# Performance work log

Measured on AMD Instinct MI355X. Metric: run time of the kernel, lower is better.

Reference implementation:

```python
import jax, jax.numpy as jnp
import numpy as np

B, S, D, H = 2, 2048, 1024, 16
HD = D // H  # 64

def setup_inputs() -> dict:
    key = jax.random.key(0)
    k1, k2, k3 = jax.random.split(key, 3)
    hidden_states = jax.random.normal(k1, (B, S, D), dtype=jnp.float32)
    w_attn = jax.random.normal(k2, (D, 3 * D), dtype=jnp.float32) * 0.02
    w_proj = jax.random.normal(k3, (D, D), dtype=jnp.float32) * 0.02
    return {"hidden_states": hidden_states, "w_attn": w_attn, "w_proj": w_proj}

def reference(hidden_states, w_attn, w_proj):
    b, s, d = hidden_states.shape
    # c_attn: Conv1D (bias is a scalar zero in the source)
    qkv = jnp.einsum('bsd,de->bse', hidden_states, w_attn)  # [B,S,3D]
    q, k, v = jnp.split(qkv, 3, axis=-1)
    def split_heads(t):
        return t.reshape(b, s, H, HD).transpose(0, 2, 1, 3)  # [B,H,S,HD]
    q, k, v = split_heads(q), split_heads(k), split_heads(v)
    # eager attention; scale_attn_weights=True -> divide by sqrt(head_dim)
    scores = jnp.einsum('bhqd,bhkd->bhqk', q, k) / jnp.sqrt(jnp.float32(HD))
    # NOTE: source registers bias buffer as all-ones (True), so the causal
    # torch.where is a no-op -- faithfully no masking is applied.
    probs = jax.nn.softmax(scores, axis=-1)
    attn = jnp.einsum('bhqk,bhkd->bhqd', probs, v)  # [B,H,S,HD]
    attn = attn.transpose(0, 2, 1, 3).reshape(b, s, d)  # merge heads
    out = jnp.einsum('bsd,de->bse', attn, w_proj)  # c_proj (zero bias)
    return out
```

## Files before the change

### kernel.cpp

```cpp
#include <hip/hip_runtime.h>
#include <hip/hip_bf16.h>

typedef __attribute__((ext_vector_type(8))) short bf16x8;
typedef __attribute__((ext_vector_type(4))) short short4v;
typedef __attribute__((ext_vector_type(4))) float f32x4;
typedef __attribute__((ext_vector_type(16))) float f32x16;
typedef __attribute__((ext_vector_type(4))) float float4v;

__device__ __forceinline__ short f2bf(float f) {
    union { float f; unsigned u; } v; v.f = f;
    unsigned r = v.u + 0x7fffu + ((v.u >> 16) & 1u);
    return (short)(r >> 16);
}
__device__ __forceinline__ float bf2f(short s) {
    union { unsigned u; float f; } v;
    v.u = ((unsigned)(unsigned short)s) << 16;
    return v.f;
}

__device__ __forceinline__ void gload16(const short* g, short* lds) {
    __builtin_amdgcn_global_load_lds(
        (const __attribute__((address_space(1))) unsigned*)g,
        (__attribute__((address_space(3))) unsigned*)lds, 16, 0, 0);
}

__device__ __forceinline__ void tconv_tile(const float* __restrict__ in,
                                           short* __restrict__ out,
                                           int Kdim, int Ndim, int n0, int k0) {
    __shared__ int Ls[64][65];
    const int t = threadIdx.x;
    const int kl = t >> 4, n4 = (t & 15) * 4;
#pragma unroll
    for (int it = 0; it < 4; ++it) {
        int k = kl + it * 16;
        float4v v = *reinterpret_cast<const float4v*>(&in[(size_t)(k0 + k) * Ndim + n0 + n4]);
#pragma unroll
        for (int c = 0; c < 4; ++c) Ls[k][n4 + c] = (int)(unsigned short)f2bf(v[c]);
    }
    __syncthreads();
    const int nl0 = t >> 4, kq = (t & 15) * 4;
#pragma unroll
    for (int it = 0; it < 4; ++it) {
        int nl = nl0 + it * 16;
        short4v s;
#pragma unroll
        for (int j = 0; j < 4; ++j) s[j] = (short)Ls[kq + j][nl];
        *reinterpret_cast<short4v*>(&out[(size_t)(n0 + nl) * Kdim + k0 + kq]) = s;
    }
}

__global__ __launch_bounds__(256) void prep1(const float* __restrict__ hidden,
                                             short* __restrict__ Ah,
                                             const float* __restrict__ w_attn,
                                             short* __restrict__ Wta) {
    const int bx = blockIdx.x;
    if (bx < 2048) {
        int i = (bx * 256 + threadIdx.x) * 8;
        float4v a0 = *reinterpret_cast<const float4v*>(&hidden[i]);
        float4v a1 = *reinterpret_cast<const float4v*>(&hidden[i + 4]);
        bf16x8 s;
        s[0] = f2bf(a0[0]); s[1] = f2bf(a0[1]); s[2] = f2bf(a0[2]); s[3] = f2bf(a0[3]);
        s[4] = f2bf(a1[0]); s[5] = f2bf(a1[1]); s[6] = f2bf(a1[2]); s[7] = f2bf(a1[3]);
        *reinterpret_cast<bf16x8*>(&Ah[i]) = s;
    } else {
        int idx = bx - 2048;
        int n0 = (idx % 48) * 64, k0 = (idx / 48) * 64;
        tconv_tile(w_attn, Wta, 1024, 3072, n0, k0);
    }
}

__global__ __launch_bounds__(256) void qkv_gemm(const short* __restrict__ Ah,
                                                const short* __restrict__ Wt,
                                                short* __restrict__ Qw,
                                                short* __restrict__ Kw,
                                                short* __restrict__ Vt) {
    __shared__ short As[128 * 64];
    __shared__ short Bs[128 * 64];
    const int tid = threadIdx.x;
    const int l = tid & 63, w = tid >> 6;
    const int g = l >> 4, lr = l & 15;
    const int r8 = l >> 3, sl = l & 7;
    const int xs = (sl ^ r8) * 8;
    const int wm = (w >> 1) * 64, wn = (w & 1) * 64;
    const int bid = blockIdx.x;
    const int xcd = bid & 7, idx = bid >> 3;
    const int nt = (xcd & 1) * 12 + idx % 12;
    const int mt = (xcd >> 1) * 8 + idx / 12;
    const int m0 = mt * 128;
    const int n0 = nt * 128;
    const bool isV = (n0 >= 2048);
    f32x4 acc[4][4] = {};
    for (int k0 = 0; k0 < 1024; k0 += 64) {
        const short* Ag = Ah + m0 * 1024 + k0;
        const short* Bg = Wt + n0 * 1024 + k0;
#pragma unroll
        for (int i = 0; i < 4; ++i) {
            int seg = w * 4 + i;
            gload16(Ag + (seg * 8 + r8) * 1024 + xs, &As[seg * 512]);
            gload16(Bg + (seg * 8 + r8) * 1024 + xs, &Bs[seg * 512]);
        }
        __syncthreads();
#pragma unroll
        for (int kk = 0; kk < 2; ++kk) {
            bf16x8 af[4], bfr[4];
#pragma unroll
            for (int mi = 0; mi < 4; ++mi) {
                int row = wm + mi * 16 + lr;
                af[mi] = *reinterpret_cast<const bf16x8*>(&As[row * 64 + (((4 * kk + g) ^ (lr & 7)) * 8)]);
            }
#pragma unroll
            for (int ni = 0; ni < 4; ++ni) {
                int col = wn + ni * 16 + lr;
                bfr[ni] = *reinterpret_cast<const bf16x8*>(&Bs[col * 64 + (((4 * kk + g) ^ (lr & 7)) * 8)]);
            }
            if (isV) {
#pragma unroll
                for (int mi = 0; mi < 4; ++mi)
#pragma unroll
                    for (int ni = 0; ni < 4; ++ni)
                        acc[mi][ni] = __builtin_amdgcn_mfma_f32_16x16x32_bf16(af[mi], bfr[ni], acc[mi][ni], 0, 0, 0);
            } else {
#pragma unroll
                for (int mi = 0; mi < 4; ++mi)
#pragma unroll
                    for (int ni = 0; ni < 4; ++ni)
                        acc[mi][ni] = __builtin_amdgcn_mfma_f32_16x16x32_bf16(bfr[ni], af[mi], acc[mi][ni], 0, 0, 0);
            }
        }
        __syncthreads();
    }
    if (isV) {
#pragma unroll
        for (int mi = 0; mi < 4; ++mi) {
            int m = m0 + wm + mi * 16 + g * 4;
            int bb = m >> 11, s0 = m & 2047;
#pragma unroll
            for (int ni = 0; ni < 4; ++ni) {
                int n = n0 + wn + ni * 16 + lr;
                int hh = (n >> 6) & 15, d = n & 63;
                short4v pv;
#pragma unroll
                for (int r = 0; r < 4; ++r) pv[r] = f2bf(acc[mi][ni][r]);
                *reinterpret_cast<short4v*>(&Vt[(((bb * 16 + hh) * 64) + d) * 2048 + s0]) = pv;
            }
        }
    } else {
        const bool isQ = (n0 < 1024);
        const float sc = isQ ? 0.18033688011112042f : 1.0f;
        short* dst = isQ ? Qw : Kw;
#pragma unroll
        for (int mi = 0; mi < 4; ++mi) {
            int m = m0 + wm + mi * 16 + lr;
            int bb = m >> 11, s0 = m & 2047;
#pragma unroll
            for (int ni = 0; ni < 4; ++ni) {
                int n = n0 + wn + ni * 16 + g * 4;
                int hh = (n >> 6) & 15, d = n & 63;
                float a0 = acc[mi][ni][0] * sc, a1 = acc[mi][ni][1] * sc;
                float a2 = acc[mi][ni][2] * sc, a3 = acc[mi][ni][3] * sc;
                int w0, w1;
                asm("v_cvt_pk_bf16_f32 %0, %1, %2" : "=v"(w0) : "v"(a0), "v"(a1));
                asm("v_cvt_pk_bf16_f32 %0, %1, %2" : "=v"(w1) : "v"(a2), "v"(a3));
                union { int wd[2]; short4v s; } u;
                u.wd[0] = w0; u.wd[1] = w1;
                *reinterpret_cast<short4v*>(&dst[((bb * 16 + hh) * 2048 + s0) * 64 + d]) = u.s;
            }
        }
    }
}

__global__ __launch_bounds__(256, 4) void attn9(const short* __restrict__ Qw,
                                                const short* __restrict__ Kw,
                                                const short* __restrict__ Vt,
                                                short* __restrict__ N0,
                                                short* __restrict__ N1,
                                                float* __restrict__ Tot) {
    __shared__ short Ks[2][64 * 64];
    __shared__ short Vs[2][64 * 64];
    const int tid = threadIdx.x;
    const int w = tid >> 6, l = tid & 63;
    const int q = l & 31, hi = l >> 5;
    const int r8 = l >> 3, sl = l & 7;
    const int xs = (sl ^ r8) * 8;
    const int bid = blockIdx.x;
    const int work = (bid & 7) * 128 + (bid >> 3);
    const int head = work >> 5;
    const int qblk = (work & 31) >> 1;
    const int ks = work & 1;
    const int b = head >> 4, h = head & 15;
    const int q0 = qblk * 128 + w * 32;
    const short* Qb = Qw + ((b * 16 + h) * 2048 + q0) * 64;
    const short* Kb = Kw + ((b * 16 + h) * 2048 + ks * 1024) * 64;
    const short* Vb = Vt + ((b * 16 + h) * 64) * 2048 + ks * 1024;

    bf16x8 qb[4];
#pragma unroll
    for (int c = 0; c < 4; ++c)
        qb[c] = *reinterpret_cast<const bf16x8*>(&Qb[q * 64 + c * 16 + hi * 8]);

    bf16x8 ones1;
#pragma unroll
    for (int j = 0; j < 8; ++j) ones1[j] = (short)0x3F80;

    int koff[2][4], voff[2][2][2];
#pragma unroll
    for (int sub = 0; sub < 2; ++sub)
#pragma unroll
        for (int c = 0; c < 4; ++c)
            koff[sub][c] = (sub * 32 + q) * 64 + (((2 * c + hi) ^ (q & 7)) * 8);
#pragma unroll
    for (int sub = 0; sub < 2; ++sub)
#pragma unroll
        for (int c2 = 0; c2 < 2; ++c2)
#pragma unroll
            for (int dt = 0; dt < 2; ++dt)
                voff[sub][c2][dt] = (dt * 32 + q) * 64 + (((4 * sub + 2 * c2 + hi) ^ (q & 7)) * 8);

    f32x16 o0 = {}, o1 = {};
    f32x16 psacc = {};

#define STAGE_KV(buf, j0)                                                        \
    {                                                                            \
        _Pragma("unroll")                                                        \
        for (int i = 0; i < 2; ++i) {                                            \
            int seg = w * 2 + i;                                                 \
            gload16(Kb + ((j0) + seg * 8 + r8) * 64 + xs, &Ks[buf][seg * 512]);  \
            gload16(Vb + (seg * 8 + r8) * 2048 + (j0) + xs, &Vs[buf][seg * 512]);\
        }                                                                        \
    }

    STAGE_KV(0, 0);
    __syncthreads();
    int cur = 0;

    for (int jt = 0; jt < 16; ++jt) {
        if (jt < 15) STAGE_KV(cur ^ 1, (jt + 1) * 64);

#pragma unroll
        for (int sub = 0; sub < 2; ++sub) {
            f32x16 st = {};
            __builtin_amdgcn_s_setprio(1);
#pragma unroll
            for (int c = 0; c < 4; ++c) {
                bf16x8 ka = *reinterpret_cast<const bf16x8*>(&Ks[cur][koff[sub][c]]);
                st = __builtin_amdgcn_mfma_f32_32x32x16_bf16(ka, qb[c], st, 0, 0, 0);
            }
            __builtin_amdgcn_s_setprio(0);
            float p[16];
#pragma unroll
            for (int r = 0; r < 16; ++r) p[r] = __builtin_amdgcn_exp2f(st[r]);
            int pk[4][2];
#pragma unroll
            for (int bq = 0; bq < 4; ++bq) {
                int w0, w1;
                asm("v_cvt_pk_bf16_f32 %0, %1, %2" : "=v"(w0) : "v"(p[4 * bq]), "v"(p[4 * bq + 1]));
                asm("v_cvt_pk_bf16_f32 %0, %1, %2" : "=v"(w1) : "v"(p[4 * bq + 2]), "v"(p[4 * bq + 3]));
                pk[bq][0] = w0; pk[bq][1] = w1;
            }
#pragma unroll
            for (int c2 = 0; c2 < 2; ++c2) {
                int w0 = pk[2 * c2][0], w2 = pk[2 * c2 + 1][0];
                int w1 = pk[2 * c2][1], w3 = pk[2 * c2 + 1][1];
                asm("v_permlane32_swap_b32 %0, %1" : "+v"(w0), "+v"(w2));
                asm("v_permlane32_swap_b32 %0, %1" : "+v"(w1), "+v"(w3));
                union { int wd[4]; bf16x8 v; } pb;
                pb.wd[0] = w0; pb.wd[1] = w1; pb.wd[2] = w2; pb.wd[3] = w3;
                __builtin_amdgcn_s_setprio(1);
                psacc = __builtin_amdgcn_mfma_f32_32x32x16_bf16(ones1, pb.v, psacc, 0, 0, 0);
#pragma unroll
                for (int dt = 0; dt < 2; ++dt) {
                    bf16x8 va = *reinterpret_cast<const bf16x8*>(&Vs[cur][voff[sub][c2][dt]]);
                    if (dt == 0) o0 = __builtin_amdgcn_mfma_f32_32x32x16_bf16(va, pb.v, o0, 0, 0, 0);
                    else         o1 = __builtin_amdgcn_mfma_f32_32x32x16_bf16(va, pb.v, o1, 0, 0, 0);
                }
                __builtin_amdgcn_s_setprio(0);
            }
        }
        __syncthreads();
        cur ^= 1;
    }
#undef STAGE_KV

    float tot = psacc[0];

    short* Nd = ks ? N1 : N0;
    short* Orow = &Nd[(b * 2048 + q0 + q) * 1024 + h * 64];
#pragma unroll
    for (int r = 0; r < 4; ++r) {
        short4v ov0, ov1;
#pragma unroll
        for (int j = 0; j < 4; ++j) {
            ov0[j] = f2bf(o0[4 * r + j]);
            ov1[j] = f2bf(o1[4 * r + j]);
        }
        *reinterpret_cast<short4v*>(&Orow[8 * r + 4 * hi]) = ov0;
        *reinterpret_cast<short4v*>(&Orow[32 + 8 * r + 4 * hi]) = ov1;
    }
    if (hi == 0)
        Tot[ks * 65536 + (b * 16 + h) * 2048 + q0 + q] = tot;
}

__global__ __launch_bounds__(256) void post(short* __restrict__ N0,
                                            const short* __restrict__ N1,
                                            const float* __restrict__ Tot,
                                            const float* __restrict__ w_proj,
                                            short* __restrict__ Wtp) {
    const int bx = blockIdx.x;
    if (bx < 2048) {
        int i = (bx * 256 + threadIdx.x) * 8;
        int bs = i >> 10;
        int b = bs >> 11, s = bs & 2047;
        int h = (i >> 6) & 15;
        int qi = (b * 16 + h) * 2048 + s;
        float t0 = Tot[qi], t1 = Tot[65536 + qi];
        float inv = 1.f / (t0 + t1);
        bf16x8 a = *reinterpret_cast<const bf16x8*>(&N0[i]);
        bf16x8 c = *reinterpret_cast<const bf16x8*>(&N1[i]);
        bf16x8 r;
#pragma unroll
        for (int j = 0; j < 8; ++j) r[j] = f2bf((bf2f(a[j]) + bf2f(c[j])) * inv);
        *reinterpret_cast<bf16x8*>(&N0[i]) = r;
    } else {
        int idx = bx - 2048;
        int n0 = (idx % 16) * 64, k0 = (idx / 16) * 64;
        tconv_tile(w_proj, Wtp, 1024, 1024, n0, k0);
    }
}

__global__ __launch_bounds__(256) void proj_gemm(const short* __restrict__ Ag,
                                                 const short* __restrict__ Wtp,
                                                 float* __restrict__ Out) {
    __shared__ short As[64 * 64];
    __shared__ short Bs[64 * 64];
    const int tid = threadIdx.x;
    const int l = tid & 63, w = tid >> 6;
    const int g = l >> 4, lr = l & 15;
    const int r8 = l >> 3, sl = l & 7;
    const int xs = (sl ^ r8) * 8;
    const int wm = (w >> 1) * 32, wn = (w & 1) * 32;
    const int bid = blockIdx.x;
    const int work = (bid & 7) * 128 + (bid >> 3);
    const int mt = work >> 4, nt = work & 15;
    const int m0 = mt * 64;
    const int n0 = nt * 64;
    f32x4 acc[2][2] = {};
    for (int k0 = 0; k0 < 1024; k0 += 64) {
        const short* Ab = Ag + m0 * 1024 + k0;
        const short* Bg = Wtp + n0 * 1024 + k0;
#pragma unroll
        for (int i = 0; i < 2; ++i) {
            int seg = w * 2 + i;
            gload16(Ab + (seg * 8 + r8) * 1024 + xs, &As[seg * 512]);
            gload16(Bg + (seg * 8 + r8) * 1024 + xs, &Bs[seg * 512]);
        }
        __syncthreads();
#pragma unroll
        for (int kk = 0; kk < 2; ++kk) {
            bf16x8 af[2], bfr[2];
#pragma unroll
            for (int mi = 0; mi < 2; ++mi) {
                int row = wm + mi * 16 + lr;
                af[mi] = *reinterpret_cast<const bf16x8*>(&As[row * 64 + (((4 * kk + g) ^ (lr & 7)) * 8)]);
            }
#pragma unroll
            for (int ni = 0; ni < 2; ++ni) {
                int col = wn + ni * 16 + lr;
                bfr[ni] = *reinterpret_cast<const bf16x8*>(&Bs[col * 64 + (((4 * kk + g) ^ (lr & 7)) * 8)]);
            }
#pragma unroll
            for (int mi = 0; mi < 2; ++mi)
#pragma unroll
                for (int ni = 0; ni < 2; ++ni)
                    acc[mi][ni] = __builtin_amdgcn_mfma_f32_16x16x32_bf16(af[mi], bfr[ni], acc[mi][ni], 0, 0, 0);
        }
        __syncthreads();
    }
#pragma unroll
    for (int mi = 0; mi < 2; ++mi) {
#pragma unroll
        for (int ni = 0; ni < 2; ++ni) {
            int n = n0 + wn + ni * 16 + lr;
#pragma unroll
            for (int r = 0; r < 4; ++r) {
                int mm = m0 + wm + mi * 16 + g * 4 + r;
                Out[mm * 1024 + n] = acc[mi][ni][r];
            }
        }
    }
}

extern "C" void kernel_launch(void* const* d_in, const int* in_sizes, int n_in,
                              void* d_out, int out_size, void* d_ws, size_t ws_size,
                              hipStream_t stream) {
    const float* hidden = (const float*)d_in[0];
    const float* w_attn = (const float*)d_in[1];
    const float* w_proj = (const float*)d_in[2];
    float* out = (float*)d_out;

    short* AhN0 = (short*)d_ws;
    short* Qw = AhN0 + 4194304;
    short* Kw = Qw + 4194304;
    short* Vt = Kw + 4194304;
    short* Wta = (short*)d_out;
    float* Tot = (float*)((char*)d_out + 7u * 1024 * 1024);
    short* N1 = (short*)((char*)d_out + 8u * 1024 * 1024);

    prep1<<<dim3(2816), 256, 0, stream>>>(hidden, AhN0, w_attn, Wta);
    qkv_gemm<<<dim3(768), 256, 0, stream>>>(AhN0, Wta, Qw, Kw, Vt);
    attn9<<<dim3(1024), 256, 0, stream>>>(Qw, Kw, Vt, AhN0, N1, Tot);
    post<<<dim3(2304), 256, 0, stream>>>(AhN0, N1, Tot, w_proj, Qw);
    proj_gemm<<<dim3(1024), 256, 0, stream>>>(AhN0, Qw, out);
}
```

Measured before the change: 119.8 us.

## Rewrite QKV GEMM with 256x256 tiles, 8 waves, double-buffered LDS prefetch

```diff
diff --git a/kernel.cpp b/kernel.cpp
--- a/kernel.cpp
+++ b/kernel.cpp
@@ -69,74 +69,115 @@
     }
 }
 
-__global__ __launch_bounds__(256) void qkv_gemm(const short* __restrict__ Ah,
-                                                const short* __restrict__ Wt,
-                                                short* __restrict__ Qw,
-                                                short* __restrict__ Kw,
-                                                short* __restrict__ Vt) {
-    __shared__ short As[128 * 64];
-    __shared__ short Bs[128 * 64];
+__global__ __launch_bounds__(512, 2) void qkv8(const short* __restrict__ Ah,
+                                               const short* __restrict__ Wt,
+                                               short* __restrict__ Qw,
+                                               short* __restrict__ Kw,
+                                               short* __restrict__ Vt) {
+    extern __shared__ short lds[];
     const int tid = threadIdx.x;
-    const int l = tid & 63, w = tid >> 6;
+    const int w = tid >> 6, l = tid & 63;
+    const int wr = w >> 2, wc = w & 3;
     const int g = l >> 4, lr = l & 15;
     const int r8 = l >> 3, sl = l & 7;
     const int xs = (sl ^ r8) * 8;
-    const int wm = (w >> 1) * 64, wn = (w & 1) * 64;
     const int bid = blockIdx.x;
     const int xcd = bid & 7, idx = bid >> 3;
-    const int nt = (xcd & 1) * 12 + idx % 12;
-    const int mt = (xcd >> 1) * 8 + idx / 12;
-    const int m0 = mt * 128;
-    const int n0 = nt * 128;
+    const int mt = (xcd >> 1) * 4 + idx / 6;
+    const int nt = (xcd & 1) * 6 + idx % 6;
+    const int m0 = mt * 256;
+    const int n0 = nt * 256;
     const bool isV = (n0 >= 2048);
-    f32x4 acc[4][4] = {};
-    for (int k0 = 0; k0 < 1024; k0 += 64) {
-        const short* Ag = Ah + m0 * 1024 + k0;
-        const short* Bg = Wt + n0 * 1024 + k0;
-#pragma unroll
-        for (int i = 0; i < 4; ++i) {
-            int seg = w * 4 + i;
-            gload16(Ag + (seg * 8 + r8) * 1024 + xs, &As[seg * 512]);
-            gload16(Bg + (seg * 8 + r8) * 1024 + xs, &Bs[seg * 512]);
-        }
-        __syncthreads();
-#pragma unroll
-        for (int kk = 0; kk < 2; ++kk) {
-            bf16x8 af[4], bfr[4];
-#pragma unroll
-            for (int mi = 0; mi < 4; ++mi) {
-                int row = wm + mi * 16 + lr;
-                af[mi] = *reinterpret_cast<const bf16x8*>(&As[row * 64 + (((4 * kk + g) ^ (lr & 7)) * 8)]);
-            }
+    f32x4 acc[8][4] = {};
+
+#define STAGE_A8(b, kt)                                                          \
+    {                                                                            \
+        const short* S = Ah + m0 * 1024 + (kt) * 64;                             \
+        _Pragma("unroll")                                                        \
+        for (int p = 0; p < 4; ++p) {                                            \
+            int seg = p * 8 + w;                                                 \
+            gload16(S + (seg * 8 + r8) * 1024 + xs, lds + (b) * 32768 + seg * 512); \
+        }                                                                        \
+    }
+#define STAGE_B8(b, kt)                                                          \
+    {                                                                            \
+        const short* S = Wt + n0 * 1024 + (kt) * 64;                             \
+        _Pragma("unroll")                                                        \
+        for (int p = 0; p < 4; ++p) {                                            \
+            int seg = p * 8 + w;                                                 \
+            gload16(S + (seg * 8 + r8) * 1024 + xs, lds + (b) * 32768 + 16384 + seg * 512); \
+        }                                                                        \
+    }
+
+    STAGE_A8(0, 0);
+    STAGE_B8(0, 0);
+    asm volatile("s_waitcnt vmcnt(0)" ::: "memory");
+    __builtin_amdgcn_s_barrier();
+
+    int cur = 0;
+    for (int kt = 0; kt < 16; ++kt) {
+        const int ao = cur * 32768;
+        const int bo = cur * 32768 + 16384;
+#pragma unroll
+        for (int qd = 0; qd < 4; ++qd) {
+            bf16x8 af[2][2], bfq[4][2];
+#pragma unroll
+            for (int j = 0; j < 2; ++j)
+#pragma unroll
+                for (int kk = 0; kk < 2; ++kk) {
+                    int row = wr * 128 + (qd * 2 + j) * 16 + lr;
+                    af[j][kk] = *reinterpret_cast<const bf16x8*>(
+                        &lds[ao + row * 64 + (((4 * kk + g) ^ (lr & 7)) * 8)]);
+                }
+#pragma unroll
+            for (int ni = 0; ni < 4; ++ni)
+#pragma unroll
+                for (int kk = 0; kk < 2; ++kk) {
+                    int row = wc * 64 + ni * 16 + lr;
+                    bfq[ni][kk] = *reinterpret_cast<const bf16x8*>(
+                        &lds[bo + row * 64 + (((4 * kk + g) ^ (lr & 7)) * 8)]);
+                }
+            if (qd == 0 && kt < 15) STAGE_A8(cur ^ 1, kt + 1);
+            if (qd == 1 && kt < 15) STAGE_B8(cur ^ 1, kt + 1);
+            __builtin_amdgcn_s_barrier();
+            __builtin_amdgcn_s_setprio(1);
+            if (isV) {
+#pragma unroll
+                for (int j = 0; j < 2; ++j)
+#pragma unroll
+                    for (int ni = 0; ni < 4; ++ni)
+#pragma unroll
+                        for (int kk = 0; kk < 2; ++kk)
+                            acc[qd * 2 + j][ni] = __builtin_amdgcn_mfma_f32_16x16x32_bf16(
+                                af[j][kk], bfq[ni][kk], acc[qd * 2 + j][ni], 0, 0, 0);
+            } else {
+#pragma unroll
+                for (int j = 0; j < 2; ++j)
+#pragma unroll
+                    for (int ni = 0; ni < 4; ++ni)
+#pragma unroll
+                        for (int kk = 0; kk < 2; ++kk)
+                            acc[qd * 2 + j][ni] = __builtin_amdgcn_mfma_f32_16x16x32_bf16(
+                                bfq[ni][kk], af[j][kk], acc[qd * 2 + j][ni], 0, 0, 0);
+            }
+            __builtin_amdgcn_s_setprio(0);
+            __builtin_amdgcn_s_barrier();
+        }
+        asm volatile("s_waitcnt vmcnt(0)" ::: "memory");
+        __builtin_amdgcn_s_barrier();
+        cur ^= 1;
+    }
+#undef STAGE_A8
+#undef STAGE_B8
+
+    if (isV) {
+#pragma unroll
+        for (int mi = 0; mi < 8; ++mi) {
+            int m = m0 + wr * 128 + mi * 16 + g * 4;
+            int bb = m >> 11, s0 = m & 2047;
 #pragma unroll
             for (int ni = 0; ni < 4; ++ni) {
-                int col = wn + ni * 16 + lr;
-                bfr[ni] = *reinterpret_cast<const bf16x8*>(&Bs[col * 64 + (((4 * kk + g) ^ (lr & 7)) * 8)]);
-            }
-            if (isV) {
-#pragma unroll
-                for (int mi = 0; mi < 4; ++mi)
-#pragma unroll
-                    for (int ni = 0; ni < 4; ++ni)
-                        acc[mi][ni] = __builtin_amdgcn_mfma_f32_16x16x32_bf16(af[mi], bfr[ni], acc[mi][ni], 0, 0, 0);
-            } else {
-#pragma unroll
-                for (int mi = 0; mi < 4; ++mi)
-#pragma unroll
-                    for (int ni = 0; ni < 4; ++ni)
-                        acc[mi][ni] = __builtin_amdgcn_mfma_f32_16x16x32_bf16(bfr[ni], af[mi], acc[mi][ni], 0, 0, 0);
-            }
-        }
-        __syncthreads();
-    }
-    if (isV) {
-#pragma unroll
-        for (int mi = 0; mi < 4; ++mi) {
-            int m = m0 + wm + mi * 16 + g * 4;
-            int bb = m >> 11, s0 = m & 2047;
-#pragma unroll
-            for (int ni = 0; ni < 4; ++ni) {
-                int n = n0 + wn + ni * 16 + lr;
+                int n = n0 + wc * 64 + ni * 16 + lr;
                 int hh = (n >> 6) & 15, d = n & 63;
                 short4v pv;
 #pragma unroll
@@ -149,12 +190,12 @@
         const float sc = isQ ? 0.18033688011112042f : 1.0f;
         short* dst = isQ ? Qw : Kw;
 #pragma unroll
-        for (int mi = 0; mi < 4; ++mi) {
-            int m = m0 + wm + mi * 16 + lr;
+        for (int mi = 0; mi < 8; ++mi) {
+            int m = m0 + wr * 128 + mi * 16 + lr;
             int bb = m >> 11, s0 = m & 2047;
 #pragma unroll
             for (int ni = 0; ni < 4; ++ni) {
-                int n = n0 + wn + ni * 16 + g * 4;
+                int n = n0 + wc * 64 + ni * 16 + g * 4;
                 int hh = (n >> 6) & 15, d = n & 63;
                 float a0 = acc[mi][ni][0] * sc, a1 = acc[mi][ni][1] * sc;
                 float a2 = acc[mi][ni][2] * sc, a3 = acc[mi][ni][3] * sc;
@@ -405,8 +446,11 @@
     float* Tot = (float*)((char*)d_out + 7u * 1024 * 1024);
     short* N1 = (short*)((char*)d_out + 8u * 1024 * 1024);
 
+    (void)hipFuncSetAttribute((const void*)qkv8,
+                              hipFuncAttributeMaxDynamicSharedMemorySize, 131072);
+
     prep1<<<dim3(2816), 256, 0, stream>>>(hidden, AhN0, w_attn, Wta);
-    qkv_gemm<<<dim3(768), 256, 0, stream>>>(AhN0, Wta, Qw, Kw, Vt);
+    qkv8<<<dim3(192), 512, 131072, stream>>>(AhN0, Wta, Qw, Kw, Vt);
     attn9<<<dim3(1024), 256, 0, stream>>>(Qw, Kw, Vt, AhN0, N1, Tot);
     post<<<dim3(2304), 256, 0, stream>>>(AhN0, N1, Tot, w_proj, Qw);
     proj_gemm<<<dim3(1024), 256, 0, stream>>>(AhN0, Qw, out);
```

Measured after the change: 127.3 us. 6.3% more time.
